# Kernel optimization log

Hardware: AMD Instinct MI355X
Metric: run time of the kernel (lower is better)

The kernel has to match this reference:

```python
import jax, jax.numpy as jnp
import numpy as np
import math

NUM_HEADS = 16

def _skew(QEr):
    # QEr: [B, H, S, S] -> pad 1 on left of last dim, reshape, drop first row
    B, H, S, _ = QEr.shape
    padded = jnp.pad(QEr, ((0, 0), (0, 0), (0, 0), (1, 0)))  # [B,H,S,S+1]
    reshaped = padded.reshape(B, H, S + 1, S)
    return reshaped[:, :, 1:, :]  # [B,H,S,S]

def setup_inputs() -> dict:
    key = jax.random.key(0)
    ks = jax.random.split(key, 8)
    B, S, D, dh = 4, 1024, 1024, 64
    x = jax.random.normal(ks[0], (B, S, D), dtype=jnp.float32)
    scale = 1.0 / math.sqrt(D)
    Wq = jax.random.normal(ks[1], (D, D), dtype=jnp.float32) * scale
    Wk = jax.random.normal(ks[2], (D, D), dtype=jnp.float32) * scale
    Wv = jax.random.normal(ks[3], (D, D), dtype=jnp.float32) * scale
    bq = jnp.zeros((D,), dtype=jnp.float32)
    bk = jnp.zeros((D,), dtype=jnp.float32)
    bv = jnp.zeros((D,), dtype=jnp.float32)
    Er = jax.random.normal(ks[4], (S, dh), dtype=jnp.float32)
    return {"x": x, "Wq": Wq, "bq": bq, "Wk": Wk, "bk": bk, "Wv": Wv, "bv": bv, "Er": Er}

def reference(x, Wq, bq, Wk, bk, Wv, bv, Er):
    B, S, D = x.shape
    H = NUM_HEADS
    dh = D // H
    # Linear projections (torch Linear: x @ W.T + b)
    q = (x @ Wq.T + bq).reshape(B, S, H, dh).transpose(0, 2, 1, 3)  # [B,H,S,dh]
    k = (x @ Wk.T + bk).reshape(B, S, H, dh).transpose(0, 2, 1, 3)
    v = (x @ Wv.T + bv).reshape(B, S, H, dh).transpose(0, 2, 1, 3)
    # Relative position term: q @ Er^T then skew (start = max_len - S = 0)
    QEr = jnp.einsum('bhsd,td->bhst', q, Er)  # [B,H,S,S]
    Srel = _skew(QEr)
    QKt = jnp.einsum('bhsd,bhtd->bhst', q, k)  # [B,H,S,S]
    attn = (QKt + Srel) / math.sqrt(dh)
    causal = jnp.tril(jnp.ones((S, S), dtype=bool))
    attn = jnp.where(causal[None, None], attn, jnp.float32(-1e6))
    attn = jax.nn.softmax(attn, axis=-1)
    out = jnp.einsum('bhst,bhtd->bhsd', attn, v)  # [B,H,S,dh]
    out = out.transpose(0, 2, 1, 3).reshape(B, S, D)
    return out  # dropout is identity in eval / p=0
```

## Files before the change

### kernel.cpp

```cpp
#include <hip/hip_runtime.h>
#include <stdint.h>

#define S_LEN 1024
#define DM 1024
#define NH 16
#define DH 64
#define NB 4

typedef unsigned short u16;
typedef __attribute__((ext_vector_type(8))) short short8;
typedef __attribute__((ext_vector_type(4))) float f32x4;
typedef __attribute__((ext_vector_type(4))) unsigned int u32x4;
typedef __attribute__((ext_vector_type(4))) unsigned short u16x4;

__device__ __forceinline__ u16 f2bf(float f) {
  union { float f; unsigned int u; } c;
  c.f = f;
  unsigned int u = c.u;
  return (u16)((u + 0x7fffu + ((u >> 16) & 1u)) >> 16);
}

__device__ __forceinline__ void g2l16(const void* g, void* l) {
  __builtin_amdgcn_global_load_lds(
      (const __attribute__((address_space(1))) unsigned int*)(uintptr_t)g,
      (__attribute__((address_space(3))) unsigned int*)(uint32_t)(uintptr_t)l,
      16, 0, 0);
}

__device__ __forceinline__ float grp16_max(float v) {
  union { float f; int i; } c, o;
  c.f = v; o.i = __builtin_amdgcn_update_dpp(c.i, c.i, 0xB1, 0xF, 0xF, false);
  v = fmaxf(v, o.f);
  c.f = v; o.i = __builtin_amdgcn_update_dpp(c.i, c.i, 0x4E, 0xF, 0xF, false);
  v = fmaxf(v, o.f);
  c.f = v; o.i = __builtin_amdgcn_update_dpp(c.i, c.i, 0x124, 0xF, 0xF, false);
  v = fmaxf(v, o.f);
  c.f = v; o.i = __builtin_amdgcn_update_dpp(c.i, c.i, 0x128, 0xF, 0xF, false);
  v = fmaxf(v, o.f);
  return v;
}
__device__ __forceinline__ float grp16_sum(float v) {
  union { float f; int i; } c, o;
  c.f = v; o.i = __builtin_amdgcn_update_dpp(c.i, c.i, 0xB1, 0xF, 0xF, false);
  v += o.f;
  c.f = v; o.i = __builtin_amdgcn_update_dpp(c.i, c.i, 0x4E, 0xF, 0xF, false);
  v += o.f;
  c.f = v; o.i = __builtin_amdgcn_update_dpp(c.i, c.i, 0x124, 0xF, 0xF, false);
  v += o.f;
  c.f = v; o.i = __builtin_amdgcn_update_dpp(c.i, c.i, 0x128, 0xF, 0xF, false);
  v += o.f;
  return v;
}

__global__ __launch_bounds__(256) void cvt_f32_bf16(
    const float* __restrict__ x, const float* __restrict__ Wq,
    const float* __restrict__ Wk, const float* __restrict__ Wv,
    const float* __restrict__ Er, u16* __restrict__ xb,
    u16* __restrict__ Wqb, u16* __restrict__ Wkb, u16* __restrict__ Wvb,
    u16* __restrict__ Erb) {
  const size_t f = ((size_t)blockIdx.x * 256 + threadIdx.x) * 8;
  const float* src;
  u16* dst;
  size_t off;
  if (f < 4194304) { src = x; dst = xb; off = f; }
  else if (f < 5242880) { src = Wq; dst = Wqb; off = f - 4194304; }
  else if (f < 6291456) { src = Wk; dst = Wkb; off = f - 5242880; }
  else if (f < 7340032) { src = Wv; dst = Wvb; off = f - 6291456; }
  else { src = Er; dst = Erb; off = f - 7340032; }
  const float4 a = *(const float4*)(src + off);
  const float4 b = *(const float4*)(src + off + 4);
  u16 o[8] = {f2bf(a.x), f2bf(a.y), f2bf(a.z), f2bf(a.w),
              f2bf(b.x), f2bf(b.y), f2bf(b.z), f2bf(b.w)};
  *(u32x4*)(dst + off) = *(const u32x4*)o;
}

__global__ __launch_bounds__(256) void qkv_gemm(
    const u16* __restrict__ x,
    const u16* __restrict__ Wq, const float* __restrict__ bq,
    const u16* __restrict__ Wk, const float* __restrict__ bk,
    const u16* __restrict__ Wv, const float* __restrict__ bv,
    u16* __restrict__ Qo, u16* __restrict__ Ko, u16* __restrict__ Vo) {
  __shared__ __attribute__((aligned(16))) u16 Al[128 * 32];
  __shared__ __attribute__((aligned(16))) u16 Bl[128 * 32];

  const int tid = threadIdx.x;
  const int lane = tid & 63;
  const int wave = tid >> 6;
  const int z = blockIdx.z;
  const u16* W = (z == 0) ? Wq : (z == 1) ? Wk : Wv;
  const float* bias = (z == 0) ? bq : (z == 1) ? bk : bv;

  const int m0 = blockIdx.y * 128;
  const int n0 = blockIdx.x * 128;

  f32x4 acc[4][4];
  const f32x4 fzero = {0.f, 0.f, 0.f, 0.f};
#pragma unroll
  for (int i = 0; i < 4; i++)
#pragma unroll
    for (int j = 0; j < 4; j++) acc[i][j] = fzero;

  const int srow = tid >> 2;
  const int schunk = tid & 3;
  const u16* gA = x + (size_t)(m0 + srow) * DM + schunk * 8;
  const u16* gB = W + (size_t)(n0 + srow) * DM + schunk * 8;

  const int fr = lane & 15;
  const int fq = lane >> 4;
  const int wr = (wave >> 1) * 64;
  const int wc = (wave & 1) * 64;

  for (int k = 0; k < DM; k += 32) {
    g2l16(gA + k, &Al[tid * 8]);
    g2l16(gA + (size_t)64 * DM + k, &Al[2048 + tid * 8]);
    g2l16(gB + k, &Bl[tid * 8]);
    g2l16(gB + (size_t)64 * DM + k, &Bl[2048 + tid * 8]);
    __syncthreads();
    short8 a[4], b[4];
#pragma unroll
    for (int i = 0; i < 4; i++)
      a[i] = *(const short8*)&Al[(wr + i * 16 + fr) * 32 + fq * 8];
#pragma unroll
    for (int j = 0; j < 4; j++)
      b[j] = *(const short8*)&Bl[(wc + j * 16 + fr) * 32 + fq * 8];
#pragma unroll
    for (int i = 0; i < 4; i++)
#pragma unroll
      for (int j = 0; j < 4; j++)
        acc[i][j] =
            __builtin_amdgcn_mfma_f32_16x16x32_bf16(a[i], b[j], acc[i][j], 0, 0, 0);
    __syncthreads();
  }

#pragma unroll
  for (int j = 0; j < 4; j++) {
    const int n = n0 + wc + j * 16 + fr;
    const float bsv = bias[n];
    const int h = n >> 6, d = n & (DH - 1);
#pragma unroll
    for (int i = 0; i < 4; i++) {
      const int mb = m0 + wr + i * 16 + fq * 4;
      const int bb = mb >> 10, s = mb & (S_LEN - 1);
      if (z == 2) {
        u16x4 o;
#pragma unroll
        for (int r = 0; r < 4; r++) o[r] = f2bf(acc[i][j][r] + bsv);
        *(u16x4*)&Vo[((size_t)(bb * NH + h) * DH + d) * S_LEN + s] = o;
      } else if (z == 1) {
#pragma unroll
        for (int r = 0; r < 4; r++)
          Ko[((size_t)(bb * NH + h) * S_LEN + s + r) * DH + d] =
              f2bf(acc[i][j][r] + bsv);
      } else {
#pragma unroll
        for (int r = 0; r < 4; r++)
          Qo[((size_t)(bb * NH + h) * S_LEN + s + r) * DH + d] =
              f2bf(acc[i][j][r] + bsv);
      }
    }
  }
}

__global__ __launch_bounds__(256, 4) void attn(
    const u16* __restrict__ Q, const u16* __restrict__ K,
    const u16* __restrict__ Vt, const u16* __restrict__ Er,
    float* __restrict__ out) {
  __shared__ __attribute__((aligned(16))) u16 Kl[64 * 64];
  __shared__ __attribute__((aligned(16))) u16 Vl[64 * 64];
  __shared__ __attribute__((aligned(16))) u16 El[128 * 64];
  __shared__ __attribute__((aligned(16))) u16 Pl[4][16 * 64];

  const int tid = threadIdx.x;
  const int lane = tid & 63;
  const int w = tid >> 6;
  const int bh = blockIdx.y;
  const int b = bh >> 4, h = bh & (NH - 1);
  const int it = ((int)blockIdx.x + bh + ((bh >> 4) << 2)) & 15;
  const int i0 = it * 64;
  const int i0w = i0 + w * 16;
  const int E0b = S_LEN - 64 - i0;

  const u16* Qb = Q + (size_t)bh * S_LEN * DH;
  const char* Kb = (const char*)(K + (size_t)bh * S_LEN * DH);
  const char* Vb = (const char*)(Vt + (size_t)bh * DH * S_LEN);
  const char* Eb = (const char*)Er;
  u16* Pw = Pl[w];

  const int fr = lane & 15;
  const int fq = lane >> 4;
  const f32x4 fzero = {0.f, 0.f, 0.f, 0.f};

  const int r8 = tid >> 3;
  const int ch = (tid & 7) * 16;

  auto stageKV = [&](int j0) {
#pragma unroll
    for (int p = 0; p < 2; p++) {
      const int row = p * 32 + r8;
      const int sw = ch ^ ((row & 7) << 4);
      g2l16(Kb + (size_t)(j0 + row) * 128 + sw, (char*)Kl + row * 128 + ch);
      g2l16(Vb + (size_t)row * 2048 + j0 * 2 + sw, (char*)Vl + row * 128 + ch);
    }
  };
  auto stageEl = [&](int e0, int np) {
    for (int p = 0; p < np; p++) {
      const int e = e0 + p * 32 + r8;
      const int slot = e & 127;
      const int ec = (e > S_LEN - 1) ? (S_LEN - 1) : e;
      const int sw = ch ^ ((slot & 7) << 4);
      g2l16(Eb + (size_t)ec * 128 + sw, (char*)El + slot * 128 + ch);
    }
  };

  const short8 aq0 = *(const short8*)&Qb[(size_t)(i0w + fr) * DH + fq * 8];
  const short8 aq1 = *(const short8*)&Qb[(size_t)(i0w + fr) * DH + 32 + fq * 8];

  float mrow[4], lp[4];
  f32x4 accO[4];
#pragma unroll
  for (int r = 0; r < 4; r++) { mrow[r] = -3.0e38f; lp[r] = 0.f; }
#pragma unroll
  for (int t = 0; t < 4; t++) accO[t] = fzero;

  f32x4 zzc = fzero;
  const int ksw = (fr & 7) << 4;

  for (int j0 = 0; j0 <= i0; j0 += 64) {
    stageKV(j0);
    if (j0 == 0) stageEl(E0b, 4);
    else stageEl(E0b + j0 + 64, 2);
    __syncthreads();

    int tmax = (i0w + 15 - j0) >> 4;
    if (tmax > 3) tmax = 3;

    f32x4 sfr[4];
#pragma unroll
    for (int t = 0; t < 4; t++) sfr[t] = fzero;
    __builtin_amdgcn_s_setprio(1);
#pragma unroll
    for (int t = 0; t < 4; t++)
      if (t <= tmax) {
        const char* kr = (const char*)Kl + (t * 16 + fr) * 128;
        const short8 b0 = *(const short8*)(kr + ((fq * 16) ^ ksw));
        const short8 b1 = *(const short8*)(kr + ((64 + fq * 16) ^ ksw));
        f32x4 z = fzero;
        z = __builtin_amdgcn_mfma_f32_16x16x32_bf16(aq0, b0, z, 0, 0, 0);
        z = __builtin_amdgcn_mfma_f32_16x16x32_bf16(aq1, b1, z, 0, 0, 0);
        sfr[t] = z;
      }
    __builtin_amdgcn_s_setprio(0);

    const int ebs = S_LEN - 16 - i0w + j0;
    f32x4 zz[5];
#pragma unroll
    for (int f = 0; f < 5; f++) zz[f] = fzero;
    const int f0 = (j0 == 0) ? 0 : 1;
#pragma unroll
    for (int f = 0; f < 5; f++)
      if (f >= f0 && f <= tmax + 1) {
        const int slot = ((ebs + f * 16) & 127) + fr;
        const char* er = (const char*)El + slot * 128;
        const short8 b0 = *(const short8*)(er + ((fq * 16) ^ ksw));
        const short8 b1 = *(const short8*)(er + ((64 + fq * 16) ^ ksw));
        f32x4 z = fzero;
        z = __builtin_amdgcn_mfma_f32_16x16x32_bf16(aq0, b0, z, 0, 0, 0);
        z = __builtin_amdgcn_mfma_f32_16x16x32_bf16(aq1, b1, z, 0, 0, 0);
        zz[f] = z;
      }
    if (j0 > 0) zz[0] = zzc;
    zzc = zz[4];

    float p[4][4];
#pragma unroll
    for (int r = 0; r < 4; r++) {
      const int row = fq * 4 + r;
      const int c = 15 - row + fr;
      const int src = (fq << 4) | (c & 15);
      float sh[5];
#pragma unroll
      for (int f = 0; f < 5; f++) sh[f] = __shfl(zz[f][r], src);
#pragma unroll
      for (int t = 0; t < 4; t++) {
        const float rel = (c < 16) ? sh[t] : sh[t + 1];
        float sv = (sfr[t][r] + rel) * 0.125f;
        const int jj = j0 + t * 16 + fr;
        const int ii = i0w + row;
        if (jj > ii) sv = -3.0e38f;
        p[t][r] = sv;
      }
    }

#pragma unroll
    for (int r = 0; r < 4; r++) {
      float rm = fmaxf(fmaxf(p[0][r], p[1][r]), fmaxf(p[2][r], p[3][r]));
      rm = grp16_max(rm);
      const float mnew = fmaxf(mrow[r], rm);
      const float alpha = __expf(mrow[r] - mnew);
      mrow[r] = mnew;
      float rs = 0.f;
#pragma unroll
      for (int t = 0; t < 4; t++) {
        const float e = __expf(p[t][r] - mnew);
        p[t][r] = e;
        rs += e;
      }
      lp[r] = lp[r] * alpha + rs;
#pragma unroll
      for (int t = 0; t < 4; t++) accO[t][r] *= alpha;
    }

#pragma unroll
    for (int t = 0; t < 4; t++)
#pragma unroll
      for (int r = 0; r < 4; r++)
        Pw[(fq * 4 + r) * 64 + (((t ^ fq) << 4) + fr)] = f2bf(p[t][r]);
    __builtin_amdgcn_s_waitcnt(0xC07F);

    const int rsw = (fr >> 2) << 4;
    const short8 ap0 = *(const short8*)&Pw[fr * 64 + ((fq * 8) ^ rsw)];
    const short8 ap1 = *(const short8*)&Pw[fr * 64 + ((32 + fq * 8) ^ rsw)];

    __builtin_amdgcn_s_setprio(1);
#pragma unroll
    for (int t = 0; t < 4; t++) {
      const char* vr = (const char*)Vl + (t * 16 + fr) * 128;
      const short8 b0 = *(const short8*)(vr + ((fq * 16) ^ ksw));
      const short8 b1 = *(const short8*)(vr + ((64 + fq * 16) ^ ksw));
      accO[t] =
          __builtin_amdgcn_mfma_f32_16x16x32_bf16(ap0, b0, accO[t], 0, 0, 0);
      accO[t] =
          __builtin_amdgcn_mfma_f32_16x16x32_bf16(ap1, b1, accO[t], 0, 0, 0);
    }
    __builtin_amdgcn_s_setprio(0);

    __syncthreads();
  }

#pragma unroll
  for (int r = 0; r < 4; r++) {
    const float lr = grp16_sum(lp[r]);
    const float inv = 1.f / lr;
    const int s = i0w + fq * 4 + r;
#pragma unroll
    for (int t = 0; t < 4; t++) {
      const int d = t * 16 + fr;
      out[((size_t)b * S_LEN + s) * DM + h * DH + d] = accO[t][r] * inv;
    }
  }
}

extern "C" void kernel_launch(void* const* d_in, const int* in_sizes, int n_in,
                              void* d_out, int out_size, void* d_ws, size_t ws_size,
                              hipStream_t stream) {
  const float* x = (const float*)d_in[0];
  const float* Wq = (const float*)d_in[1];
  const float* bq = (const float*)d_in[2];
  const float* Wk = (const float*)d_in[3];
  const float* bk = (const float*)d_in[4];
  const float* Wv = (const float*)d_in[5];
  const float* bv = (const float*)d_in[6];
  const float* Er = (const float*)d_in[7];
  float* out = (float*)d_out;

  const size_t per = (size_t)NB * NH * S_LEN * DH;
  u16* Qw = (u16*)d_ws;
  u16* Kw = Qw + per;
  u16* Vw = Kw + per;
  u16* xb = Vw + per;
  u16* Wqb = xb + per;
  u16* Wkb = Wqb + (size_t)DM * DM;
  u16* Wvb = Wkb + (size_t)DM * DM;
  u16* Erb = Wvb + (size_t)DM * DM;

  cvt_f32_bf16<<<3616, 256, 0, stream>>>(x, Wq, Wk, Wv, Er, xb, Wqb, Wkb, Wvb,
                                         Erb);
  dim3 g1(DM / 128, (NB * S_LEN) / 128, 3);
  qkv_gemm<<<g1, dim3(256), 0, stream>>>(xb, Wqb, bq, Wkb, bk, Wvb, bv, Qw, Kw,
                                         Vw);
  dim3 g2(16, NB * NH);
  attn<<<g2, dim3(256), 0, stream>>>(Qw, Kw, Vw, Erb, out);
}
```

Measured before the change: 185.5 us.

## Double-buffer K/V in attention, use 128-row query tiles, swizzle QKV GEMM blocks

The attention kernel now runs 512 threads (8 waves) per block, so each block covers 128 query rows and the K/V/Er tiles it loads are shared by twice as many rows. K and V are double-buffered so the next tile's global-to-LDS load is issued before the current tile is computed. The Er ring grows to 256 rows and is staged one 64-row chunk per step. Query-tile order is reversed for half the heads to even out causal load. Separately, the QKV GEMM remaps its flat block index so consecutive blocks share A/B tiles in cache. The cost is more LDS per block and fewer, larger blocks, which lowers occupancy and parallelism (512 attention blocks instead of 1024).

```diff
diff --git a/kernel.cpp b/kernel.cpp
--- a/kernel.cpp
+++ b/kernel.cpp
@@ -86,12 +86,17 @@
   const int tid = threadIdx.x;
   const int lane = tid & 63;
   const int wave = tid >> 6;
-  const int z = blockIdx.z;
+
+  const int o =
+      ((int)blockIdx.z * gridDim.y + blockIdx.y) * gridDim.x + blockIdx.x;
+  const int swz = (o & 7) * 96 + (o >> 3);
+  const int z = swz >> 8;
+  const int rem = swz & 255;
+  const int m0 = (rem >> 3) * 128;
+  const int n0 = (rem & 7) * 128;
+
   const u16* W = (z == 0) ? Wq : (z == 1) ? Wk : Wv;
   const float* bias = (z == 0) ? bq : (z == 1) ? bk : bv;
-
-  const int m0 = blockIdx.y * 128;
-  const int n0 = blockIdx.x * 128;
 
   f32x4 acc[4][4];
   const f32x4 fzero = {0.f, 0.f, 0.f, 0.f};
@@ -142,10 +147,10 @@
       const int mb = m0 + wr + i * 16 + fq * 4;
       const int bb = mb >> 10, s = mb & (S_LEN - 1);
       if (z == 2) {
-        u16x4 o;
-#pragma unroll
-        for (int r = 0; r < 4; r++) o[r] = f2bf(acc[i][j][r] + bsv);
-        *(u16x4*)&Vo[((size_t)(bb * NH + h) * DH + d) * S_LEN + s] = o;
+        u16x4 ov;
+#pragma unroll
+        for (int r = 0; r < 4; r++) ov[r] = f2bf(acc[i][j][r] + bsv);
+        *(u16x4*)&Vo[((size_t)(bb * NH + h) * DH + d) * S_LEN + s] = ov;
       } else if (z == 1) {
 #pragma unroll
         for (int r = 0; r < 4; r++)
@@ -161,24 +166,25 @@
   }
 }
 
-__global__ __launch_bounds__(256, 4) void attn(
+__global__ __launch_bounds__(512, 4) void attn(
     const u16* __restrict__ Q, const u16* __restrict__ K,
     const u16* __restrict__ Vt, const u16* __restrict__ Er,
     float* __restrict__ out) {
-  __shared__ __attribute__((aligned(16))) u16 Kl[64 * 64];
-  __shared__ __attribute__((aligned(16))) u16 Vl[64 * 64];
-  __shared__ __attribute__((aligned(16))) u16 El[128 * 64];
-  __shared__ __attribute__((aligned(16))) u16 Pl[4][16 * 64];
+  __shared__ __attribute__((aligned(16))) u16 Kl[2][64 * 64];
+  __shared__ __attribute__((aligned(16))) u16 Vl[2][64 * 64];
+  __shared__ __attribute__((aligned(16))) u16 El[256 * 64];
+  __shared__ __attribute__((aligned(16))) u16 Pl[8][16 * 64];
 
   const int tid = threadIdx.x;
   const int lane = tid & 63;
   const int w = tid >> 6;
   const int bh = blockIdx.y;
   const int b = bh >> 4, h = bh & (NH - 1);
-  const int it = ((int)blockIdx.x + bh + ((bh >> 4) << 2)) & 15;
-  const int i0 = it * 64;
+  const int it = (bh < 32) ? (int)blockIdx.x : 7 - (int)blockIdx.x;
+  const int i0 = it * 128;
+  const int jmax = i0 + 64;
   const int i0w = i0 + w * 16;
-  const int E0b = S_LEN - 64 - i0;
+  const int E0b = S_LEN - 128 - i0;
 
   const u16* Qb = Q + (size_t)bh * S_LEN * DH;
   const char* Kb = (const char*)(K + (size_t)bh * S_LEN * DH);
@@ -190,22 +196,19 @@
   const int fq = lane >> 4;
   const f32x4 fzero = {0.f, 0.f, 0.f, 0.f};
 
-  const int r8 = tid >> 3;
+  const int r0 = tid >> 3;
   const int ch = (tid & 7) * 16;
 
-  auto stageKV = [&](int j0) {
-#pragma unroll
-    for (int p = 0; p < 2; p++) {
-      const int row = p * 32 + r8;
-      const int sw = ch ^ ((row & 7) << 4);
-      g2l16(Kb + (size_t)(j0 + row) * 128 + sw, (char*)Kl + row * 128 + ch);
-      g2l16(Vb + (size_t)row * 2048 + j0 * 2 + sw, (char*)Vl + row * 128 + ch);
-    }
+  auto stageKV = [&](int j0, int bf) {
+    const int sw = ch ^ ((r0 & 7) << 4);
+    g2l16(Kb + (size_t)(j0 + r0) * 128 + sw, (char*)&Kl[bf][0] + r0 * 128 + ch);
+    g2l16(Vb + (size_t)r0 * 2048 + j0 * 2 + sw,
+          (char*)&Vl[bf][0] + r0 * 128 + ch);
   };
   auto stageEl = [&](int e0, int np) {
     for (int p = 0; p < np; p++) {
-      const int e = e0 + p * 32 + r8;
-      const int slot = e & 127;
+      const int e = e0 + p * 64 + r0;
+      const int slot = e & 255;
       const int ec = (e > S_LEN - 1) ? (S_LEN - 1) : e;
       const int sw = ch ^ ((slot & 7) << 4);
       g2l16(Eb + (size_t)ec * 128 + sw, (char*)El + slot * 128 + ch);
@@ -225,116 +228,124 @@
   f32x4 zzc = fzero;
   const int ksw = (fr & 7) << 4;
 
-  for (int j0 = 0; j0 <= i0; j0 += 64) {
-    stageKV(j0);
-    if (j0 == 0) stageEl(E0b, 4);
-    else stageEl(E0b + j0 + 64, 2);
-    __syncthreads();
+  int buf = 0;
+  stageKV(0, 0);
+  stageEl(E0b, 3);
+  __syncthreads();
+
+  for (int j0 = 0; j0 <= jmax; j0 += 64) {
+    if (j0 < jmax) {
+      stageKV(j0 + 64, buf ^ 1);
+      stageEl(E0b + j0 + 192, 1);
+    }
 
     int tmax = (i0w + 15 - j0) >> 4;
     if (tmax > 3) tmax = 3;
 
-    f32x4 sfr[4];
-#pragma unroll
-    for (int t = 0; t < 4; t++) sfr[t] = fzero;
-    __builtin_amdgcn_s_setprio(1);
-#pragma unroll
-    for (int t = 0; t < 4; t++)
-      if (t <= tmax) {
-        const char* kr = (const char*)Kl + (t * 16 + fr) * 128;
-        const short8 b0 = *(const short8*)(kr + ((fq * 16) ^ ksw));
-        const short8 b1 = *(const short8*)(kr + ((64 + fq * 16) ^ ksw));
-        f32x4 z = fzero;
-        z = __builtin_amdgcn_mfma_f32_16x16x32_bf16(aq0, b0, z, 0, 0, 0);
-        z = __builtin_amdgcn_mfma_f32_16x16x32_bf16(aq1, b1, z, 0, 0, 0);
-        sfr[t] = z;
+    if (tmax >= 0) {
+      f32x4 sfr[4];
+#pragma unroll
+      for (int t = 0; t < 4; t++) sfr[t] = fzero;
+      __builtin_amdgcn_s_setprio(1);
+#pragma unroll
+      for (int t = 0; t < 4; t++)
+        if (t <= tmax) {
+          const char* kr = (const char*)&Kl[buf][0] + (t * 16 + fr) * 128;
+          const short8 b0 = *(const short8*)(kr + ((fq * 16) ^ ksw));
+          const short8 b1 = *(const short8*)(kr + ((64 + fq * 16) ^ ksw));
+          f32x4 z = fzero;
+          z = __builtin_amdgcn_mfma_f32_16x16x32_bf16(aq0, b0, z, 0, 0, 0);
+          z = __builtin_amdgcn_mfma_f32_16x16x32_bf16(aq1, b1, z, 0, 0, 0);
+          sfr[t] = z;
+        }
+      __builtin_amdgcn_s_setprio(0);
+
+      const int ebs = S_LEN - 16 - i0w + j0;
+      f32x4 zz[5];
+#pragma unroll
+      for (int f = 0; f < 5; f++) zz[f] = fzero;
+      const int f0 = (j0 == 0) ? 0 : 1;
+#pragma unroll
+      for (int f = 0; f < 5; f++)
+        if (f >= f0 && f <= tmax + 1) {
+          const int slot = ((ebs + f * 16) & 255) + fr;
+          const char* er = (const char*)El + slot * 128;
+          const short8 b0 = *(const short8*)(er + ((fq * 16) ^ ksw));
+          const short8 b1 = *(const short8*)(er + ((64 + fq * 16) ^ ksw));
+          f32x4 z = fzero;
+          z = __builtin_amdgcn_mfma_f32_16x16x32_bf16(aq0, b0, z, 0, 0, 0);
+          z = __builtin_amdgcn_mfma_f32_16x16x32_bf16(aq1, b1, z, 0, 0, 0);
+          zz[f] = z;
+        }
+      if (j0 > 0) zz[0] = zzc;
+      zzc = zz[4];
+
+      float p[4][4];
+#pragma unroll
+      for (int r = 0; r < 4; r++) {
+        const int row = fq * 4 + r;
+        const int c = 15 - row + fr;
+        const int src = (fq << 4) | (c & 15);
+        float sh[5];
+#pragma unroll
+        for (int f = 0; f < 5; f++) sh[f] = __shfl(zz[f][r], src);
+#pragma unroll
+        for (int t = 0; t < 4; t++) {
+          const float rel = (c < 16) ? sh[t] : sh[t + 1];
+          float sv = (sfr[t][r] + rel) * 0.125f;
+          const int jj = j0 + t * 16 + fr;
+          const int ii = i0w + row;
+          if (jj > ii) sv = -3.0e38f;
+          p[t][r] = sv;
+        }
       }
-    __builtin_amdgcn_s_setprio(0);
-
-    const int ebs = S_LEN - 16 - i0w + j0;
-    f32x4 zz[5];
-#pragma unroll
-    for (int f = 0; f < 5; f++) zz[f] = fzero;
-    const int f0 = (j0 == 0) ? 0 : 1;
-#pragma unroll
-    for (int f = 0; f < 5; f++)
-      if (f >= f0 && f <= tmax + 1) {
-        const int slot = ((ebs + f * 16) & 127) + fr;
-        const char* er = (const char*)El + slot * 128;
-        const short8 b0 = *(const short8*)(er + ((fq * 16) ^ ksw));
-        const short8 b1 = *(const short8*)(er + ((64 + fq * 16) ^ ksw));
-        f32x4 z = fzero;
-        z = __builtin_amdgcn_mfma_f32_16x16x32_bf16(aq0, b0, z, 0, 0, 0);
-        z = __builtin_amdgcn_mfma_f32_16x16x32_bf16(aq1, b1, z, 0, 0, 0);
-        zz[f] = z;
+
+#pragma unroll
+      for (int r = 0; r < 4; r++) {
+        float rm = fmaxf(fmaxf(p[0][r], p[1][r]), fmaxf(p[2][r], p[3][r]));
+        rm = grp16_max(rm);
+        const float mnew = fmaxf(mrow[r], rm);
+        const float alpha = __expf(mrow[r] - mnew);
+        mrow[r] = mnew;
+        float rs = 0.f;
+#pragma unroll
+        for (int t = 0; t < 4; t++) {
+          const float e = __expf(p[t][r] - mnew);
+          p[t][r] = e;
+          rs += e;
+        }
+        lp[r] = lp[r] * alpha + rs;
+#pragma unroll
+        for (int t = 0; t < 4; t++) accO[t][r] *= alpha;
       }
-    if (j0 > 0) zz[0] = zzc;
-    zzc = zz[4];
-
-    float p[4][4];
-#pragma unroll
-    for (int r = 0; r < 4; r++) {
-      const int row = fq * 4 + r;
-      const int c = 15 - row + fr;
-      const int src = (fq << 4) | (c & 15);
-      float sh[5];
-#pragma unroll
-      for (int f = 0; f < 5; f++) sh[f] = __shfl(zz[f][r], src);
+
+#pragma unroll
+      for (int t = 0; t < 4; t++)
+#pragma unroll
+        for (int r = 0; r < 4; r++)
+          Pw[(fq * 4 + r) * 64 + (((t ^ fq) << 4) + fr)] = f2bf(p[t][r]);
+      __builtin_amdgcn_s_waitcnt(0xC07F);
+
+      const int rsw = (fr >> 2) << 4;
+      const short8 ap0 = *(const short8*)&Pw[fr * 64 + ((fq * 8) ^ rsw)];
+      const short8 ap1 = *(const short8*)&Pw[fr * 64 + ((32 + fq * 8) ^ rsw)];
+
+      __builtin_amdgcn_s_setprio(1);
 #pragma unroll
       for (int t = 0; t < 4; t++) {
-        const float rel = (c < 16) ? sh[t] : sh[t + 1];
-        float sv = (sfr[t][r] + rel) * 0.125f;
-        const int jj = j0 + t * 16 + fr;
-        const int ii = i0w + row;
-        if (jj > ii) sv = -3.0e38f;
-        p[t][r] = sv;
+        const char* vr = (const char*)&Vl[buf][0] + (t * 16 + fr) * 128;
+        const short8 b0 = *(const short8*)(vr + ((fq * 16) ^ ksw));
+        const short8 b1 = *(const short8*)(vr + ((64 + fq * 16) ^ ksw));
+        accO[t] =
+            __builtin_amdgcn_mfma_f32_16x16x32_bf16(ap0, b0, accO[t], 0, 0, 0);
+        accO[t] =
+            __builtin_amdgcn_mfma_f32_16x16x32_bf16(ap1, b1, accO[t], 0, 0, 0);
       }
-    }
-
-#pragma unroll
-    for (int r = 0; r < 4; r++) {
-      float rm = fmaxf(fmaxf(p[0][r], p[1][r]), fmaxf(p[2][r], p[3][r]));
-      rm = grp16_max(rm);
-      const float mnew = fmaxf(mrow[r], rm);
-      const float alpha = __expf(mrow[r] - mnew);
-      mrow[r] = mnew;
-      float rs = 0.f;
-#pragma unroll
-      for (int t = 0; t < 4; t++) {
-        const float e = __expf(p[t][r] - mnew);
-        p[t][r] = e;
-        rs += e;
-      }
-      lp[r] = lp[r] * alpha + rs;
-#pragma unroll
-      for (int t = 0; t < 4; t++) accO[t][r] *= alpha;
-    }
-
-#pragma unroll
-    for (int t = 0; t < 4; t++)
-#pragma unroll
-      for (int r = 0; r < 4; r++)
-        Pw[(fq * 4 + r) * 64 + (((t ^ fq) << 4) + fr)] = f2bf(p[t][r]);
-    __builtin_amdgcn_s_waitcnt(0xC07F);
-
-    const int rsw = (fr >> 2) << 4;
-    const short8 ap0 = *(const short8*)&Pw[fr * 64 + ((fq * 8) ^ rsw)];
-    const short8 ap1 = *(const short8*)&Pw[fr * 64 + ((32 + fq * 8) ^ rsw)];
-
-    __builtin_amdgcn_s_setprio(1);
-#pragma unroll
-    for (int t = 0; t < 4; t++) {
-      const char* vr = (const char*)Vl + (t * 16 + fr) * 128;
-      const short8 b0 = *(const short8*)(vr + ((fq * 16) ^ ksw));
-      const short8 b1 = *(const short8*)(vr + ((64 + fq * 16) ^ ksw));
-      accO[t] =
-          __builtin_amdgcn_mfma_f32_16x16x32_bf16(ap0, b0, accO[t], 0, 0, 0);
-      accO[t] =
-          __builtin_amdgcn_mfma_f32_16x16x32_bf16(ap1, b1, accO[t], 0, 0, 0);
-    }
-    __builtin_amdgcn_s_setprio(0);
+      __builtin_amdgcn_s_setprio(0);
+    }
 
     __syncthreads();
+    buf ^= 1;
   }
 
 #pragma unroll
@@ -378,6 +389,6 @@
   dim3 g1(DM / 128, (NB * S_LEN) / 128, 3);
   qkv_gemm<<<g1, dim3(256), 0, stream>>>(xb, Wqb, bq, Wkb, bk, Wvb, bv, Qw, Kw,
                                          Vw);
-  dim3 g2(16, NB * NH);
-  attn<<<g2, dim3(256), 0, stream>>>(Qw, Kw, Vw, Erb, out);
-}
+  dim3 g2(8, NB * NH);
+  attn<<<g2, dim3(512), 0, stream>>>(Qw, Kw, Vw, Erb, out);
+}
```

Result: faster. 175.8 us (-5.2%).
